# Optimization experiments

Hardware: AMD Instinct MI355X
Metric: run time of the kernel (lower is better)

The kernel has to match this reference:

```python
import jax, jax.numpy as jnp
import numpy as np

HIDDEN = 1024
N_HEAD = 16
HEAD_DIM = HIDDEN // N_HEAD


def _rope(x):
    # x: [b, h, l, d]; interleaved RoPE, matching the torch module exactly
    L, d = x.shape[-2], x.shape[-1]
    pos = jnp.arange(L, dtype=x.dtype)[:, None]                      # [L, 1]
    ids = jnp.arange(d // 2, dtype=x.dtype)
    theta = jnp.power(jnp.asarray(10000.0, x.dtype), 2.0 * ids / d)  # [d/2]
    ang = pos / theta                                                # [L, d/2]
    sin = jnp.repeat(jnp.sin(ang), 2, axis=-1)                       # [L, d]
    cos = jnp.repeat(jnp.cos(ang), 2, axis=-1)                       # [L, d]
    # rotate pairs: (x0, x1) -> (-x1, x0)
    x_rot = jnp.stack([-x[..., 1::2], x[..., 0::2]], axis=-1).reshape(x.shape)
    return x * cos + x_rot * sin


def setup_inputs() -> dict:
    key = jax.random.key(0)
    ks = jax.random.split(key, 5)
    B, LQ, LK = 8, 1024, 2048
    scale = 1.0 / np.sqrt(HIDDEN)
    return {
        "x": jax.random.normal(ks[0], (B, LQ, HIDDEN), dtype=jnp.float32),
        "y": jax.random.normal(ks[1], (B, LK, HIDDEN), dtype=jnp.float32),
        "Wq": jax.random.normal(ks[2], (HIDDEN, HIDDEN), dtype=jnp.float32) * scale,
        "Wkv": jax.random.normal(ks[3], (2 * HIDDEN, HIDDEN), dtype=jnp.float32) * scale,
        "Wo": jax.random.normal(ks[4], (HIDDEN, HIDDEN), dtype=jnp.float32) * scale,
    }


def reference(x, y, Wq, Wkv, Wo):
    B, LQ, _ = x.shape
    LK = y.shape[1]
    # projections (torch Linear: out = in @ W.T)
    q = (x @ Wq.T).reshape(B, LQ, N_HEAD, HEAD_DIM).transpose(0, 2, 1, 3)   # [b,h,lq,d]
    kv = (y @ Wkv.T).reshape(B, LK, N_HEAD, 2 * HEAD_DIM).transpose(0, 2, 1, 3)
    k, v = jnp.split(kv, 2, axis=-1)                                         # [b,h,lk,d] each
    q = _rope(q)
    k = _rope(k)
    # NOTE: the original forward does NOT apply self.scale, no dropout, no mask (eval mode)
    scores = jnp.einsum("bhqd,bhkd->bhqk", q, k)
    probs = jax.nn.softmax(scores, axis=-1)
    out = jnp.einsum("bhqk,bhkd->bhqd", probs, v)
    out = out.transpose(0, 2, 1, 3).reshape(B, LQ, HIDDEN)
    return out @ Wo.T
```

## Files before the change

### kernel.cpp

```cpp
#include <hip/hip_runtime.h>

typedef _Float16 f16;
typedef __attribute__((ext_vector_type(8))) _Float16 f16x8;
typedef __attribute__((ext_vector_type(4))) _Float16 f16x4;
typedef __attribute__((ext_vector_type(4))) float f32x4;

constexpr int B_ = 8, LQ = 1024, LK = 2048, NH = 16, HID = 1024;

__device__ __forceinline__ void gll16(const void* g, void* l) {
  __builtin_amdgcn_global_load_lds((const __attribute__((address_space(1))) void*)g,
                                   (__attribute__((address_space(3))) void*)l, 16, 0, 0);
}

__global__ __launch_bounds__(256) void cvt_f32_f16(const float* __restrict__ src,
                                                   f16* __restrict__ dst, int n4) {
  int t = blockIdx.x * 256 + threadIdx.x;
  if (t >= n4) return;
  float4 v = ((const float4*)src)[t];
  f16x4 o = {(f16)v.x, (f16)v.y, (f16)v.z, (f16)v.w};
  ((f16x4*)dst)[t] = o;
}

template <int MODE>
__global__ __launch_bounds__(256) void gemm_fused(const f16* __restrict__ A,
                                                  const f16* __restrict__ Bm,
                                                  void* __restrict__ out0,
                                                  void* __restrict__ out1,
                                                  int M, int N, int K) {
  const int n0 = blockIdx.x * 128, m0 = blockIdx.y * 128;
  const int tid = threadIdx.x, lane = tid & 63, w = tid >> 6;
  const int wm = w >> 1, wn = w & 1;
  const int quad = lane >> 4, l16 = lane & 15;
  __shared__ __align__(16) f16 As[128 * 64];
  __shared__ __align__(16) f16 Bs[128 * 64];
  f32x4 acc[4][4] = {};
  const int sr = tid >> 3, sc = (tid & 7) * 8;
  const f16* ga = A + (size_t)(m0 + sr) * K + sc;
  const f16* gb = Bm + (size_t)(n0 + sr) * K + sc;
  for (int k0 = 0; k0 < K; k0 += 64) {
    __syncthreads();
#pragma unroll
    for (int p = 0; p < 4; ++p) {
      gll16(ga + (size_t)p * 32 * K + k0, &As[(sr + p * 32) * 64 + sc]);
      gll16(gb + (size_t)p * 32 * K + k0, &Bs[(sr + p * 32) * 64 + sc]);
    }
    __syncthreads();
#pragma unroll
    for (int ks = 0; ks < 2; ++ks) {
      f16x8 af[4], bfr[4];
#pragma unroll
      for (int i = 0; i < 4; ++i) {
        af[i] = *(const f16x8*)&As[(wm * 64 + i * 16 + l16) * 64 + ks * 32 + quad * 8];
        bfr[i] = *(const f16x8*)&Bs[(wn * 64 + i * 16 + l16) * 64 + ks * 32 + quad * 8];
      }
#pragma unroll
      for (int i = 0; i < 4; ++i)
#pragma unroll
        for (int j = 0; j < 4; ++j)
          acc[i][j] = __builtin_amdgcn_mfma_f32_16x16x32_f16(af[i], bfr[j], acc[i][j], 0, 0, 0);
    }
  }
  if (MODE == 2) {
#pragma unroll
    for (int i = 0; i < 4; ++i)
#pragma unroll
      for (int j = 0; j < 4; ++j) {
        int row = m0 + wm * 64 + i * 16 + quad * 4;
        int col = n0 + wn * 64 + j * 16 + l16;
#pragma unroll
        for (int r = 0; r < 4; ++r)
          ((float*)out0)[(size_t)(row + r) * N + col] = acc[i][j][r];
      }
    return;
  }
  constexpr int LSH = (MODE == 0) ? 10 : 11;
  constexpr int LMSK = (MODE == 0) ? 1023 : 2047;
  const int Ltok = LMSK + 1;
  if (MODE == 0 || wn == 0) {
#pragma unroll
    for (int j = 0; j < 4; ++j) {
      int c = n0 + wn * 64 + j * 16 + l16;
      int h = (MODE == 0) ? (c >> 6) : (n0 >> 7);
      int d = (MODE == 0) ? (c & 63) : (j * 16 + l16);
      float inv_t = exp2f((float)(d >> 1) * -0.41524101186091903f);
#pragma unroll
      for (int i = 0; i < 4; ++i) {
        f32x4 v = acc[i][j];
        f32x4 pv;
#pragma unroll
        for (int r = 0; r < 4; ++r) pv[r] = __shfl_xor(v[r], 1, 64);
        int row0 = m0 + wm * 64 + i * 16 + quad * 4;
#pragma unroll
        for (int r = 0; r < 4; ++r) {
          int row = row0 + r;
          int pos = row & LMSK, b = row >> LSH;
          float ang = (float)pos * inv_t;
          float sn, cs;
          __sincosf(ang, &sn, &cs);
          float o = (d & 1) ? (v[r] * cs + pv[r] * sn) : (v[r] * cs - pv[r] * sn);
          int dsw = (MODE == 1) ? (d ^ ((pos & 7) << 3)) : d;
          ((f16*)out0)[(((size_t)b * NH + h) * Ltok + pos) * 64 + dsw] = (f16)o;
        }
      }
    }
  } else {
    const int h = n0 >> 7;
#pragma unroll
    for (int j = 0; j < 4; ++j) {
      int dv = j * 16 + l16;
#pragma unroll
      for (int i = 0; i < 4; ++i) {
        int row0 = m0 + wm * 64 + i * 16 + quad * 4;
        int pos0 = row0 & 2047, b = row0 >> 11;
        int kc = pos0 >> 6, klo = pos0 & 63;
        f32x4 v = acc[i][j];
        f16x4 pk = {(f16)v[0], (f16)v[1], (f16)v[2], (f16)v[3]};
        int klosw = klo ^ ((dv & 7) << 3);
        *(f16x4*)&((f16*)out1)[((((size_t)b * NH + h) * 32 + kc) * 64 + dv) * 64 + klosw] = pk;
      }
    }
  }
}

__global__ __launch_bounds__(256, 4) void attn(const f16* __restrict__ Qb,
                                               const f16* __restrict__ Kb,
                                               const f16* __restrict__ Vt,
                                               f16* __restrict__ attnb) {
  const int bh = blockIdx.x, b = bh >> 4, h = bh & 15;
  const int q0 = blockIdx.y * 128;
  const int tid = threadIdx.x, lane = tid & 63, w = tid >> 6;
  const int quad = lane >> 4, l16 = lane & 15;
  const int sw = (l16 & 7) << 3;
  __shared__ __align__(16) f16 Ks[64 * 64];
  __shared__ __align__(16) f16 Vts[64 * 64];
  const f16* qptr = Qb + ((size_t)bh * LQ + q0 + 32 * w + l16) * 64;
  f16x8 qf[2][2];
#pragma unroll
  for (int qs = 0; qs < 2; ++qs) {
    qf[qs][0] = *(const f16x8*)&qptr[qs * 16 * 64 + quad * 8];
    qf[qs][1] = *(const f16x8*)&qptr[qs * 16 * 64 + 32 + quad * 8];
  }
  const f16x4 ones4 = {(f16)1.f, (f16)1.f, (f16)1.f, (f16)1.f};
  f32x4 o[2][4] = {};
  f32x4 lacc[2] = {};
  float m_run[2] = {-1e30f, -1e30f};
  const f16* kbase = Kb + (size_t)bh * LK * 64;
  const f16* vtb = Vt + (size_t)bh * 32 * 4096;
  const int sr = tid >> 3, sc = (tid & 7) * 8;
  for (int c = 0; c < LK / 64; ++c) {
    __syncthreads();
    gll16(kbase + (size_t)(c * 64 + sr) * 64 + sc, &Ks[sr * 64 + sc]);
    gll16(kbase + (size_t)(c * 64 + sr + 32) * 64 + sc, &Ks[(sr + 32) * 64 + sc]);
    gll16(vtb + (size_t)(c * 64 + sr) * 64 + sc, &Vts[sr * 64 + sc]);
    gll16(vtb + (size_t)(c * 64 + sr + 32) * 64 + sc, &Vts[(sr + 32) * 64 + sc]);
    __syncthreads();
    f32x4 sacc[2][4] = {};
#pragma unroll
    for (int nt = 0; nt < 4; ++nt) {
      const f16* krow = &Ks[(nt * 16 + l16) * 64];
      f16x8 kf0 = *(const f16x8*)&krow[(quad * 8) ^ sw];
      f16x8 kf1 = *(const f16x8*)&krow[(32 + quad * 8) ^ sw];
#pragma unroll
      for (int qs = 0; qs < 2; ++qs) {
        sacc[qs][nt] = __builtin_amdgcn_mfma_f32_16x16x32_f16(kf0, qf[qs][0], sacc[qs][nt], 0, 0, 0);
        sacc[qs][nt] = __builtin_amdgcn_mfma_f32_16x16x32_f16(kf1, qf[qs][1], sacc[qs][nt], 0, 0, 0);
      }
    }
    f16x4 pb[2][4];
#pragma unroll
    for (int qs = 0; qs < 2; ++qs) {
      float mx = sacc[qs][0][0];
#pragma unroll
      for (int nt = 0; nt < 4; ++nt)
#pragma unroll
        for (int r = 0; r < 4; ++r) mx = fmaxf(mx, sacc[qs][nt][r]);
      mx = fmaxf(mx, __shfl_xor(mx, 16, 64));
      mx = fmaxf(mx, __shfl_xor(mx, 32, 64));
      if (!__all(mx <= m_run[qs] + 8.0f)) {
        float mn = fmaxf(m_run[qs], mx);
        float al = __expf(m_run[qs] - mn);
        m_run[qs] = mn;
#pragma unroll
        for (int r = 0; r < 4; ++r) lacc[qs][r] *= al;
#pragma unroll
        for (int dt = 0; dt < 4; ++dt)
#pragma unroll
          for (int r = 0; r < 4; ++r) o[qs][dt][r] *= al;
      }
      float m = m_run[qs];
#pragma unroll
      for (int nt = 0; nt < 4; ++nt) {
        f16x4 p;
#pragma unroll
        for (int r = 0; r < 4; ++r) p[r] = (f16)__expf(sacc[qs][nt][r] - m);
        pb[qs][nt] = p;
        lacc[qs] = __builtin_amdgcn_mfma_f32_16x16x16f16(ones4, p, lacc[qs], 0, 0, 0);
      }
    }
#pragma unroll
    for (int dt = 0; dt < 4; ++dt)
#pragma unroll
      for (int nt = 0; nt < 4; ++nt) {
        f16x4 vf = *(const f16x4*)&Vts[(dt * 16 + l16) * 64 + ((nt * 16 + quad * 4) ^ sw)];
#pragma unroll
        for (int qs = 0; qs < 2; ++qs)
          o[qs][dt] = __builtin_amdgcn_mfma_f32_16x16x16f16(vf, pb[qs][nt], o[qs][dt], 0, 0, 0);
      }
  }
#pragma unroll
  for (int qs = 0; qs < 2; ++qs) {
    float inv = 1.0f / lacc[qs][0];
    int q = q0 + 32 * w + qs * 16 + l16;
#pragma unroll
    for (int dt = 0; dt < 4; ++dt) {
      f16x4 ov;
#pragma unroll
      for (int r = 0; r < 4; ++r) ov[r] = (f16)(o[qs][dt][r] * inv);
      *(f16x4*)&attnb[((size_t)b * LQ + q) * HID + h * 64 + dt * 16 + quad * 4] = ov;
    }
  }
}

extern "C" void kernel_launch(void* const* d_in, const int* in_sizes, int n_in,
                              void* d_out, int out_size, void* d_ws, size_t ws_size,
                              hipStream_t stream) {
  const float* x = (const float*)d_in[0];
  const float* y = (const float*)d_in[1];
  const float* Wq = (const float*)d_in[2];
  const float* Wkv = (const float*)d_in[3];
  const float* Wo = (const float*)d_in[4];
  float* out = (float*)d_out;

  char* p = (char*)d_ws;
  f16* xb = (f16*)p;    p += (size_t)B_ * LQ * HID * 2;
  f16* yb = (f16*)p;    p += (size_t)B_ * LK * HID * 2;
  f16* Wqb = (f16*)p;   p += (size_t)HID * HID * 2;
  f16* Wkvb = (f16*)p;  p += (size_t)2 * HID * HID * 2;
  f16* Wob = (f16*)p;   p += (size_t)HID * HID * 2;
  f16* Qb = (f16*)p;    p += (size_t)B_ * LQ * HID * 2;
  f16* Kb = (f16*)p;    p += (size_t)B_ * LK * HID * 2;
  f16* Vt = (f16*)p;    p += (size_t)B_ * LK * HID * 2;
  f16* attnb = xb;

  auto cvt = [&](const float* s, f16* d, size_t n) {
    cvt_f32_f16<<<dim3((unsigned)((n / 4 + 255) / 256)), 256, 0, stream>>>(s, d, (int)(n / 4));
  };
  cvt(x, xb, (size_t)B_ * LQ * HID);
  cvt(y, yb, (size_t)B_ * LK * HID);
  cvt(Wq, Wqb, (size_t)HID * HID);
  cvt(Wkv, Wkvb, (size_t)2 * HID * HID);
  cvt(Wo, Wob, (size_t)HID * HID);

  gemm_fused<0><<<dim3(HID / 128, B_ * LQ / 128), 256, 0, stream>>>(
      xb, Wqb, Qb, nullptr, B_ * LQ, HID, HID);
  gemm_fused<1><<<dim3(2 * HID / 128, B_ * LK / 128), 256, 0, stream>>>(
      yb, Wkvb, Kb, Vt, B_ * LK, 2 * HID, HID);

  attn<<<dim3(B_ * NH, LQ / 128), 256, 0, stream>>>(Qb, Kb, Vt, attnb);

  gemm_fused<2><<<dim3(HID / 128, B_ * LQ / 128), 256, 0, stream>>>(
      attnb, Wob, out, nullptr, B_ * LQ, HID, HID);
}
```

Baseline: 422.7 us.

## Double-buffer LDS tiles and remap workgroups for XCD-aware locality

Both the GEMM and attention kernels now use two LDS buffers, prefetching the next K-tile through global_load_lds while the current one is computed, with one wait+barrier per iteration instead of two syncthreads. Workgroup IDs are remapped so consecutive logical tiles land on the same XCD (round-robin by 8), aiming to improve L2 reuse of shared operands such as K/V per head. MFMA sections get raised wave priority. LDS use doubles, which may reduce occupancy; the attention kernel keeps its launch bound of 4 blocks per CU.

```diff
diff --git a/kernel.cpp b/kernel.cpp
--- a/kernel.cpp
+++ b/kernel.cpp
@@ -27,38 +27,62 @@
                                                   void* __restrict__ out0,
                                                   void* __restrict__ out1,
                                                   int M, int N, int K) {
-  const int n0 = blockIdx.x * 128, m0 = blockIdx.y * 128;
+  const int gx = gridDim.x;
+  const int nwg = gx * gridDim.y;
+  const int cpx = nwg >> 3;
+  const int fid = blockIdx.y * gx + blockIdx.x;
+  const int lid = (fid & 7) * cpx + (fid >> 3);
+  const int n0 = (lid % gx) * 128, m0 = (lid / gx) * 128;
   const int tid = threadIdx.x, lane = tid & 63, w = tid >> 6;
   const int wm = w >> 1, wn = w & 1;
   const int quad = lane >> 4, l16 = lane & 15;
-  __shared__ __align__(16) f16 As[128 * 64];
-  __shared__ __align__(16) f16 Bs[128 * 64];
+  __shared__ __align__(16) f16 As[2][128 * 64];
+  __shared__ __align__(16) f16 Bs[2][128 * 64];
   f32x4 acc[4][4] = {};
   const int sr = tid >> 3, sc = (tid & 7) * 8;
   const f16* ga = A + (size_t)(m0 + sr) * K + sc;
   const f16* gb = Bm + (size_t)(n0 + sr) * K + sc;
-  for (int k0 = 0; k0 < K; k0 += 64) {
-    __syncthreads();
+  const int NT = K >> 6;
+
+  auto STAGE = [&](int t) {
+    f16* as = As[t & 1];
+    f16* bs = Bs[t & 1];
+    const int k0 = t << 6;
 #pragma unroll
     for (int p = 0; p < 4; ++p) {
-      gll16(ga + (size_t)p * 32 * K + k0, &As[(sr + p * 32) * 64 + sc]);
-      gll16(gb + (size_t)p * 32 * K + k0, &Bs[(sr + p * 32) * 64 + sc]);
-    }
-    __syncthreads();
+      gll16(ga + (size_t)p * 32 * K + k0, &as[(sr + p * 32) * 64 + sc]);
+      gll16(gb + (size_t)p * 32 * K + k0, &bs[(sr + p * 32) * 64 + sc]);
+    }
+  };
+
+  STAGE(0);
+  asm volatile("s_waitcnt vmcnt(0)" ::: "memory");
+  __builtin_amdgcn_s_barrier();
+  __builtin_amdgcn_sched_barrier(0);
+
+  for (int t = 0; t < NT; ++t) {
+    if (t + 1 < NT) STAGE(t + 1);
+    const f16* as = As[t & 1];
+    const f16* bs = Bs[t & 1];
 #pragma unroll
     for (int ks = 0; ks < 2; ++ks) {
       f16x8 af[4], bfr[4];
 #pragma unroll
       for (int i = 0; i < 4; ++i) {
-        af[i] = *(const f16x8*)&As[(wm * 64 + i * 16 + l16) * 64 + ks * 32 + quad * 8];
-        bfr[i] = *(const f16x8*)&Bs[(wn * 64 + i * 16 + l16) * 64 + ks * 32 + quad * 8];
-      }
+        af[i] = *(const f16x8*)&as[(wm * 64 + i * 16 + l16) * 64 + ks * 32 + quad * 8];
+        bfr[i] = *(const f16x8*)&bs[(wn * 64 + i * 16 + l16) * 64 + ks * 32 + quad * 8];
+      }
+      __builtin_amdgcn_s_setprio(1);
 #pragma unroll
       for (int i = 0; i < 4; ++i)
 #pragma unroll
         for (int j = 0; j < 4; ++j)
           acc[i][j] = __builtin_amdgcn_mfma_f32_16x16x32_f16(af[i], bfr[j], acc[i][j], 0, 0, 0);
-    }
+      __builtin_amdgcn_s_setprio(0);
+    }
+    asm volatile("s_waitcnt vmcnt(0)" ::: "memory");
+    __builtin_amdgcn_s_barrier();
+    __builtin_amdgcn_sched_barrier(0);
   }
   if (MODE == 2) {
 #pragma unroll
@@ -126,13 +150,15 @@
                                                const f16* __restrict__ Kb,
                                                const f16* __restrict__ Vt,
                                                f16* __restrict__ attnb) {
-  const int bh = blockIdx.x, b = bh >> 4, h = bh & 15;
-  const int q0 = blockIdx.y * 128;
+  const int fid = blockIdx.x;
+  const int lid = (fid & 7) * 128 + (fid >> 3);
+  const int bh = lid >> 3, b = bh >> 4, h = bh & 15;
+  const int q0 = (lid & 7) * 128;
   const int tid = threadIdx.x, lane = tid & 63, w = tid >> 6;
   const int quad = lane >> 4, l16 = lane & 15;
   const int sw = (l16 & 7) << 3;
-  __shared__ __align__(16) f16 Ks[64 * 64];
-  __shared__ __align__(16) f16 Vts[64 * 64];
+  __shared__ __align__(16) f16 Ks[2][64 * 64];
+  __shared__ __align__(16) f16 Vts[2][64 * 64];
   const f16* qptr = Qb + ((size_t)bh * LQ + q0 + 32 * w + l16) * 64;
   f16x8 qf[2][2];
 #pragma unroll
@@ -147,17 +173,30 @@
   const f16* kbase = Kb + (size_t)bh * LK * 64;
   const f16* vtb = Vt + (size_t)bh * 32 * 4096;
   const int sr = tid >> 3, sc = (tid & 7) * 8;
-  for (int c = 0; c < LK / 64; ++c) {
-    __syncthreads();
-    gll16(kbase + (size_t)(c * 64 + sr) * 64 + sc, &Ks[sr * 64 + sc]);
-    gll16(kbase + (size_t)(c * 64 + sr + 32) * 64 + sc, &Ks[(sr + 32) * 64 + sc]);
-    gll16(vtb + (size_t)(c * 64 + sr) * 64 + sc, &Vts[sr * 64 + sc]);
-    gll16(vtb + (size_t)(c * 64 + sr + 32) * 64 + sc, &Vts[(sr + 32) * 64 + sc]);
-    __syncthreads();
+
+  auto STAGE = [&](int c) {
+    f16* ks = Ks[c & 1];
+    f16* vs = Vts[c & 1];
+    gll16(kbase + (size_t)(c * 64 + sr) * 64 + sc, &ks[sr * 64 + sc]);
+    gll16(kbase + (size_t)(c * 64 + sr + 32) * 64 + sc, &ks[(sr + 32) * 64 + sc]);
+    gll16(vtb + (size_t)(c * 64 + sr) * 64 + sc, &vs[sr * 64 + sc]);
+    gll16(vtb + (size_t)(c * 64 + sr + 32) * 64 + sc, &vs[(sr + 32) * 64 + sc]);
+  };
+
+  constexpr int NC = LK / 64;
+  STAGE(0);
+  asm volatile("s_waitcnt vmcnt(0)" ::: "memory");
+  __builtin_amdgcn_s_barrier();
+  __builtin_amdgcn_sched_barrier(0);
+
+  for (int c = 0; c < NC; ++c) {
+    if (c + 1 < NC) STAGE(c + 1);
+    const f16* Ksb = Ks[c & 1];
+    const f16* Vsb = Vts[c & 1];
     f32x4 sacc[2][4] = {};
 #pragma unroll
     for (int nt = 0; nt < 4; ++nt) {
-      const f16* krow = &Ks[(nt * 16 + l16) * 64];
+      const f16* krow = &Ksb[(nt * 16 + l16) * 64];
       f16x8 kf0 = *(const f16x8*)&krow[(quad * 8) ^ sw];
       f16x8 kf1 = *(const f16x8*)&krow[(32 + quad * 8) ^ sw];
 #pragma unroll
@@ -201,11 +240,14 @@
     for (int dt = 0; dt < 4; ++dt)
 #pragma unroll
       for (int nt = 0; nt < 4; ++nt) {
-        f16x4 vf = *(const f16x4*)&Vts[(dt * 16 + l16) * 64 + ((nt * 16 + quad * 4) ^ sw)];
+        f16x4 vf = *(const f16x4*)&Vsb[(dt * 16 + l16) * 64 + ((nt * 16 + quad * 4) ^ sw)];
 #pragma unroll
         for (int qs = 0; qs < 2; ++qs)
           o[qs][dt] = __builtin_amdgcn_mfma_f32_16x16x16f16(vf, pb[qs][nt], o[qs][dt], 0, 0, 0);
       }
+    asm volatile("s_waitcnt vmcnt(0)" ::: "memory");
+    __builtin_amdgcn_s_barrier();
+    __builtin_amdgcn_sched_barrier(0);
   }
 #pragma unroll
   for (int qs = 0; qs < 2; ++qs) {
@@ -256,7 +298,7 @@
   gemm_fused<1><<<dim3(2 * HID / 128, B_ * LK / 128), 256, 0, stream>>>(
       yb, Wkvb, Kb, Vt, B_ * LK, 2 * HID, HID);
 
-  attn<<<dim3(B_ * NH, LQ / 128), 256, 0, stream>>>(Qb, Kb, Vt, attnb);
+  attn<<<dim3(B_ * NH * (LQ / 128)), 256, 0, stream>>>(Qb, Kb, Vt, attnb);
 
   gemm_fused<2><<<dim3(HID / 128, B_ * LQ / 128), 256, 0, stream>>>(
       attnb, Wob, out, nullptr, B_ * LQ, HID, HID);
```

Measured after the change: 414.1 us. 2.0% less time.
